# Optimization experiments

Measured on AMD Instinct MI355X. Metric: run time of the kernel, lower is better.

Reference implementation:

```python
import jax, jax.numpy as jnp
import numpy as np

B, T, DIM, H = 2, 2048, 1024, 16
DH = DIM // H  # head dim = 64, rope half = 32


def _apply_rope(q, k):
    # q,k: [b,h,t,d]
    b, h, t, d = q.shape
    half = d // 2
    idx = jnp.arange(half, dtype=jnp.float32)
    pos = jnp.arange(t, dtype=jnp.float32)[:, None]
    inv = 10000.0 ** (-2.0 * idx / (2.0 * half))
    ang = pos * inv  # [t, half]
    cos = jnp.cos(ang).astype(q.dtype)[None, None]  # [1,1,t,half]
    sin = jnp.sin(ang).astype(q.dtype)[None, None]

    def rot(x):
        a = x[..., :half]
        b2 = x[..., half:2 * half]
        return jnp.concatenate([a * cos - b2 * sin, a * sin + b2 * cos], axis=-1)

    return rot(q), rot(k)


def setup_inputs() -> dict:
    key = jax.random.key(0)
    k0, k1, k2 = jax.random.split(key, 3)
    x = jax.random.normal(k0, (B, T, DIM), dtype=jnp.float32)
    mask = jnp.tril(jnp.ones((T, T), dtype=jnp.int32))[None, None]  # causal [1,1,T,T]
    scale = DIM ** -0.5
    W_qkv = jax.random.normal(k1, (DIM, 3 * DIM), dtype=jnp.float32) * scale
    b_qkv = jnp.zeros((3 * DIM,), dtype=jnp.float32)
    W_out = jax.random.normal(k2, (DIM, DIM), dtype=jnp.float32) * scale
    b_out = jnp.zeros((DIM,), dtype=jnp.float32)
    return {"x": x, "mask": mask, "W_qkv": W_qkv, "b_qkv": b_qkv,
            "W_out": W_out, "b_out": b_out}


def reference(x, mask, W_qkv, b_qkv, W_out, b_out):
    b, t, c = x.shape
    qkv = x @ W_qkv + b_qkv  # [b,t,3c]
    q, k, v = jnp.split(qkv, 3, axis=-1)
    q = q.reshape(b, t, H, DH).transpose(0, 2, 1, 3)  # [b,h,t,dh]
    k = k.reshape(b, t, H, DH).transpose(0, 2, 1, 3)
    v = v.reshape(b, t, H, DH).transpose(0, 2, 1, 3)
    q, k = _apply_rope(q, k)
    s = jnp.einsum('bhqd,bhkd->bhqk', q, k) * (DH ** -0.5)
    s = jnp.where(mask == 0, -jnp.inf, s)
    p = jax.nn.softmax(s, axis=-1)  # dropout is identity (drop=0.0)
    y = jnp.einsum('bhqk,bhkd->bhqd', p, v)
    y = y.transpose(0, 2, 1, 3).reshape(b, t, c)
    return y @ W_out + b_out
```

## Files before the change

kernel.cpp:

```cpp
#include <hip/hip_runtime.h>
#include <hip/hip_bf16.h>
#include <math.h>

#define BB 2
#define TT 2048
#define DIMM 1024
#define HH 16
#define DHH 64

typedef _Float16 half8_t __attribute__((ext_vector_type(8)));
typedef _Float16 half4_t __attribute__((ext_vector_type(4)));
typedef float floatx4 __attribute__((ext_vector_type(4)));

typedef const unsigned int __attribute__((address_space(1)))* gp_t;
typedef unsigned int __attribute__((address_space(3)))* lp_t;

__device__ __forceinline__ void async16(const void* g, void* l) {
    __builtin_amdgcn_global_load_lds((gp_t)g, (lp_t)l, 16, 0, 0);
}

template <int CTRL>
__device__ __forceinline__ float dppmov(float x) {
    return __builtin_bit_cast(float, __builtin_amdgcn_update_dpp(
        0, __builtin_bit_cast(int, x), CTRL, 0xf, 0xf, false));
}
__device__ __forceinline__ float rowred_sum(float v) {
    v += dppmov<0x128>(v);
    v += dppmov<0x124>(v);
    v += dppmov<0x122>(v);
    v += dppmov<0x121>(v);
    return v;
}

__global__ __launch_bounds__(256) void prep_kernel(
    const float* __restrict__ x, _Float16* __restrict__ xb,
    const float* __restrict__ W_qkv, _Float16* __restrict__ Wqt,
    const float* __restrict__ W_out, _Float16* __restrict__ Wot,
    float2* __restrict__ tab) {
    __shared__ float tile[32][33];
    int bid = blockIdx.x, tid = threadIdx.x;
    if (bid < 4096) {
        int i = (bid * 256 + tid) * 4;
        floatx4 v = *(const floatx4*)(x + i);
        half4_t h;
        h[0] = (_Float16)v[0]; h[1] = (_Float16)v[1];
        h[2] = (_Float16)v[2]; h[3] = (_Float16)v[3];
        *(half4_t*)(xb + i) = h;
    } else if (bid < 8192) {
        const float* W; _Float16* Wt; int K, N, bx, by;
        if (bid < 7168) {
            W = W_qkv; Wt = Wqt; K = 1024; N = 3072;
            int b2 = bid - 4096; bx = b2 % 96; by = b2 / 96;
        } else {
            W = W_out; Wt = Wot; K = 1024; N = 1024;
            int b2 = bid - 7168; bx = b2 & 31; by = b2 >> 5;
        }
        int n0 = bx * 32, k0 = by * 32;
        int tx = tid & 31, ty = tid >> 5;
        for (int i = 0; i < 32; i += 8)
            tile[ty + i][tx] = W[(size_t)(k0 + ty + i) * N + n0 + tx];
        __syncthreads();
        for (int i = 0; i < 32; i += 8)
            Wt[(size_t)(n0 + ty + i) * K + k0 + tx] = (_Float16)tile[tx][ty + i];
    } else {
        int idx = (bid - 8192) * 256 + tid;
        int t = idx >> 5, d = idx & 31;
        float inv = __expf(-(float)d * 0.28782313662425572f);
        float ang = (float)t * inv;
        float s, c;
        __sincosf(ang, &s, &c);
        tab[idx] = make_float2(c, s);
    }
}

template <int BN, int MODE>
__global__ __launch_bounds__(256) void gemm_ld_kernel(
    const _Float16* __restrict__ A, const _Float16* __restrict__ Bt,
    const float* __restrict__ bias, float* __restrict__ C,
    _Float16* __restrict__ Qr, _Float16* __restrict__ Kr, _Float16* __restrict__ Vt,
    const float2* __restrict__ tab,
    int M, int N, int K) {
    constexpr int NB = (BN == 128) ? 4 : 2;
    constexpr int BCH = BN * 32;
    constexpr int BOFF = 3 * 4096;
    __shared__ __align__(16) _Float16 smem[3 * 4096 + 3 * BCH];
    int tid = threadIdx.x;
    int m0 = blockIdx.y * 128, n0 = blockIdx.x * BN;
    int wave = tid >> 6, lane = tid & 63;
    int wm = (wave & 1) * 64;
    int wn = (wave >> 1) * (BN / 2);
    int lm = lane & 15, quad = lane >> 4;

    floatx4 acc[4][NB] = {};

    int arow = tid >> 2, ach = tid & 3;
    int acol = ((ach ^ (arow & 3)) << 3);

    auto stage = [&](int k0, int buf) {
        _Float16* Ab = smem + buf * 4096;
        _Float16* Bb = smem + BOFF + buf * BCH;
        async16(A + (size_t)(m0 + arow) * K + k0 + acol, (char*)Ab + tid * 16);
        async16(A + (size_t)(m0 + 64 + arow) * K + k0 + acol, (char*)Ab + (256 + tid) * 16);
        async16(Bt + (size_t)(n0 + arow) * K + k0 + acol, (char*)Bb + tid * 16);
        if (BN == 128)
            async16(Bt + (size_t)(n0 + 64 + arow) * K + k0 + acol, (char*)Bb + (256 + tid) * 16);
    };

    int nIt = K >> 5;
    stage(0, 0);
    stage(32, 1);
    int fsw = (quad ^ (lm & 3)) << 3;
    for (int it = 0; it < nIt; ++it) {
        int buf = it % 3;
        if (it < nIt - 1) {
            if (BN == 128) asm volatile("s_waitcnt vmcnt(4)" ::: "memory");
            else           asm volatile("s_waitcnt vmcnt(3)" ::: "memory");
        } else {
            asm volatile("s_waitcnt vmcnt(0)" ::: "memory");
        }
        asm volatile("s_barrier" ::: "memory");
        if (it + 2 < nIt) stage((it + 2) << 5, (it + 2) % 3);

        const _Float16* Ab = smem + buf * 4096;
        const _Float16* Bb = smem + BOFF + buf * BCH;
        half8_t af[4], bf[NB];
        for (int mb = 0; mb < 4; mb++)
            af[mb] = *(const half8_t*)&Ab[(wm + mb * 16 + lm) * 32 + fsw];
        for (int nb = 0; nb < NB; nb++)
            bf[nb] = *(const half8_t*)&Bb[(wn + nb * 16 + lm) * 32 + fsw];
        for (int mb = 0; mb < 4; mb++)
            for (int nb = 0; nb < NB; nb++)
                acc[mb][nb] = __builtin_amdgcn_mfma_f32_16x16x32_f16(af[mb], bf[nb], acc[mb][nb], 0, 0, 0);
    }

    if (MODE == 0) {
        for (int mb = 0; mb < 4; mb++) {
            int row = m0 + wm + mb * 16 + quad * 4;
            for (int nb = 0; nb < NB; nb++) {
                int col = n0 + wn + nb * 16 + lm;
                float bv = bias[col];
                for (int r = 0; r < 4; r++)
                    C[(size_t)(row + r) * N + col] = acc[mb][nb][r] + bv;
            }
        }
    } else {
        __syncthreads();
        _Float16* scratch = smem + wave * 4096;
        int col0 = n0 + wn;
        int sect = col0 >> 10;
        int h = (col0 & 1023) >> 6;
        int b = (m0 + wm) >> 11;
        int tbase = (m0 + wm) & 2047;
        if (sect < 2) {
            _Float16* dst = (sect == 0) ? Qr : Kr;
            float fscale = (sect == 0) ? 0.18033688011112042f : 1.0f;
            for (int nb = 0; nb < 2; nb++) {
                int d = nb * 16 + lm;
                float bva = bias[col0 + d];
                float bvb = bias[col0 + d + 32];
                int d2 = d + 32;
                for (int mb = 0; mb < 4; mb++) {
                    for (int r = 0; r < 4; r++) {
                        int tl = mb * 16 + quad * 4 + r;
                        float2 cs = tab[(tbase + tl) * 32 + d];
                        float va = acc[mb][nb][r] + bva;
                        float vb = acc[mb][nb + 2][r] + bvb;
                        int sw = tl & 7;
                        scratch[tl * 64 + (((d >> 3) ^ sw) << 3) + (d & 7)] =
                            (_Float16)((va * cs.x - vb * cs.y) * fscale);
                        scratch[tl * 64 + (((d2 >> 3) ^ sw) << 3) + (d2 & 7)] =
                            (_Float16)((va * cs.y + vb * cs.x) * fscale);
                    }
                }
            }
            asm volatile("s_waitcnt lgkmcnt(0)" ::: "memory");
            size_t ob = (size_t)(b * HH + h) * TT + tbase;
            for (int j = 0; j < 8; j++) {
                int row = j * 8 + (lane >> 3);
                int c = lane & 7;
                half8_t v = *(const half8_t*)&scratch[row * 64 + ((c ^ (row & 7)) << 3)];
                *(half8_t*)&dst[(ob + row) * 64 + c * 8] = v;
            }
        } else {
            for (int nb = 0; nb < 4; nb++) {
                int d = nb * 16 + lm;
                float bv = bias[col0 + d];
                int sw = d & 7;
                for (int mb = 0; mb < 4; mb++) {
                    int t0 = mb * 16 + quad * 4;
                    half4_t pv;
                    for (int r = 0; r < 4; r++) pv[r] = (_Float16)(acc[mb][nb][r] + bv);
                    *(half4_t*)&scratch[d * 64 + (((t0 >> 3) ^ sw) << 3) + (t0 & 7)] = pv;
                }
            }
            asm volatile("s_waitcnt lgkmcnt(0)" ::: "memory");
            size_t vb0 = (size_t)(b * HH + h) * 64;
            for (int j = 0; j < 8; j++) {
                int drow = j * 8 + (lane >> 3);
                int c = lane & 7;
                half8_t v = *(const half8_t*)&scratch[drow * 64 + ((c ^ (drow & 7)) << 3)];
                *(half8_t*)&Vt[(vb0 + drow) * TT + tbase + c * 8] = v;
            }
        }
    }
}

__global__ __launch_bounds__(512, 2) void qkv_gemm256(
    const _Float16* __restrict__ A, const _Float16* __restrict__ Bt,
    const float* __restrict__ bias,
    _Float16* __restrict__ Qr, _Float16* __restrict__ Kr, _Float16* __restrict__ Vt,
    const float2* __restrict__ tab) {
    constexpr int K = 1024;
    __shared__ __align__(16) _Float16 smem[65536];
    int tid = threadIdx.x;
    int m0 = blockIdx.y * 256, n0 = blockIdx.x * 256;
    int wave = tid >> 6, lane = tid & 63;
    int wm = (wave & 1) * 128;
    int wn = (wave >> 1) * 64;
    int lm = lane & 15, quad = lane >> 4;

    int srow = tid >> 3;
    int sch = (tid & 7) ^ (srow & 7);
    const _Float16* aSrc = A + (size_t)(m0 + srow) * K + sch * 8;
    const _Float16* bSrc = Bt + (size_t)(n0 + srow) * K + sch * 8;

    auto stageA = [&](int kt, int buf) {
        const _Float16* s = aSrc + kt * 64;
        char* d = (char*)smem + buf * 32768 + tid * 16;
#pragma unroll
        for (int i = 0; i < 4; i++)
            async16(s + (size_t)i * 64 * K, d + i * 8192);
    };
    auto stageB = [&](int kt, int buf) {
        const _Float16* s = bSrc + kt * 64;
        char* d = (char*)smem + 65536 + buf * 32768 + tid * 16;
#pragma unroll
        for (int i = 0; i < 4; i++)
            async16(s + (size_t)i * 64 * K, d + i * 8192);
    };

    int ch0 = (quad ^ (lm & 7)) << 3;
    int ch1 = ((4 + quad) ^ (lm & 7)) << 3;

    floatx4 acc[8][4] = {};
    half8_t af[4][2], bf[4][2];

    stageA(0, 0);
    stageB(0, 0);
    asm volatile("s_waitcnt vmcnt(0)" ::: "memory");
    __builtin_amdgcn_s_barrier();

#pragma unroll 2
    for (int kt = 0; kt < 16; ++kt) {
        int c = kt & 1, nbuf = c ^ 1;
        const _Float16* Ap = smem + c * 16384 + (wm + lm) * 64;
        const _Float16* Bp = smem + 32768 + c * 16384 + (wn + lm) * 64;

#pragma unroll
        for (int mf = 0; mf < 4; mf++) {
            af[mf][0] = *(const half8_t*)(Ap + mf * 1024 + ch0);
            af[mf][1] = *(const half8_t*)(Ap + mf * 1024 + ch1);
        }
#pragma unroll
        for (int nf = 0; nf < 2; nf++) {
            bf[nf][0] = *(const half8_t*)(Bp + nf * 1024 + ch0);
            bf[nf][1] = *(const half8_t*)(Bp + nf * 1024 + ch1);
        }
        if (kt < 15) stageA(kt + 1, nbuf);
        __builtin_amdgcn_s_barrier();
        __builtin_amdgcn_s_setprio(1);
#pragma unroll
        for (int mf = 0; mf < 4; mf++)
#pragma unroll
            for (int nf = 0; nf < 2; nf++) {
                acc[mf][nf] = __builtin_amdgcn_mfma_f32_16x16x32_f16(af[mf][0], bf[nf][0], acc[mf][nf], 0, 0, 0);
                acc[mf][nf] = __builtin_amdgcn_mfma_f32_16x16x32_f16(af[mf][1], bf[nf][1], acc[mf][nf], 0, 0, 0);
            }
        __builtin_amdgcn_s_setprio(0);
        __builtin_amdgcn_s_barrier();

#pragma unroll
        for (int nf = 2; nf < 4; nf++) {
            bf[nf][0] = *(const half8_t*)(Bp + nf * 1024 + ch0);
            bf[nf][1] = *(const half8_t*)(Bp + nf * 1024 + ch1);
        }
        if (kt < 15) stageB(kt + 1, nbuf);
        __builtin_amdgcn_s_barrier();
        __builtin_amdgcn_s_setprio(1);
#pragma unroll
        for (int mf = 0; mf < 4; mf++)
#pragma unroll
            for (int nf = 2; nf < 4; nf++) {
                acc[mf][nf] = __builtin_amdgcn_mfma_f32_16x16x32_f16(af[mf][0], bf[nf][0], acc[mf][nf], 0, 0, 0);
                acc[mf][nf] = __builtin_amdgcn_mfma_f32_16x16x32_f16(af[mf][1], bf[nf][1], acc[mf][nf], 0, 0, 0);
            }
        __builtin_amdgcn_s_setprio(0);
        __builtin_amdgcn_s_barrier();

#pragma unroll
        for (int mf = 0; mf < 4; mf++) {
            af[mf][0] = *(const half8_t*)(Ap + (4 + mf) * 1024 + ch0);
            af[mf][1] = *(const half8_t*)(Ap + (4 + mf) * 1024 + ch1);
        }
        __builtin_amdgcn_s_barrier();
        __builtin_amdgcn_s_setprio(1);
#pragma unroll
        for (int mf = 0; mf < 4; mf++)
#pragma unroll
            for (int nf = 2; nf < 4; nf++) {
                acc[4 + mf][nf] = __builtin_amdgcn_mfma_f32_16x16x32_f16(af[mf][0], bf[nf][0], acc[4 + mf][nf], 0, 0, 0);
                acc[4 + mf][nf] = __builtin_amdgcn_mfma_f32_16x16x32_f16(af[mf][1], bf[nf][1], acc[4 + mf][nf], 0, 0, 0);
            }
        __builtin_amdgcn_s_setprio(0);
        __builtin_amdgcn_s_barrier();

        __builtin_amdgcn_s_setprio(1);
#pragma unroll
        for (int mf = 0; mf < 4; mf++)
#pragma unroll
            for (int nf = 0; nf < 2; nf++) {
                acc[4 + mf][nf] = __builtin_amdgcn_mfma_f32_16x16x32_f16(af[mf][0], bf[nf][0], acc[4 + mf][nf], 0, 0, 0);
                acc[4 + mf][nf] = __builtin_amdgcn_mfma_f32_16x16x32_f16(af[mf][1], bf[nf][1], acc[4 + mf][nf], 0, 0, 0);
            }
        __builtin_amdgcn_s_setprio(0);
        asm volatile("s_waitcnt vmcnt(0)" ::: "memory");
        __builtin_amdgcn_s_barrier();
    }

    __syncthreads();
    _Float16* scratch = smem + wave * 8192;
    int col0 = n0 + wn;
    int sect = col0 >> 10;
    int h = (col0 & 1023) >> 6;
    int b = (m0 + wm) >> 11;
    int tbase = (m0 + wm) & 2047;
    if (sect < 2) {
        _Float16* dst = (sect == 0) ? Qr : Kr;
        float fscale = (sect == 0) ? 0.18033688011112042f : 1.0f;
#pragma unroll
        for (int nb = 0; nb < 2; nb++) {
            int d = nb * 16 + lm;
            float bva = bias[col0 + d];
            float bvb = bias[col0 + d + 32];
            int d2 = d + 32;
#pragma unroll
            for (int mf = 0; mf < 8; mf++) {
#pragma unroll
                for (int r = 0; r < 4; r++) {
                    int tl = mf * 16 + quad * 4 + r;
                    float2 cs = tab[(tbase + tl) * 32 + d];
                    float va = acc[mf][nb][r] + bva;
                    float vb = acc[mf][nb + 2][r] + bvb;
                    int sw = tl & 7;
                    scratch[tl * 64 + (((d >> 3) ^ sw) << 3) + (d & 7)] =
                        (_Float16)((va * cs.x - vb * cs.y) * fscale);
                    scratch[tl * 64 + (((d2 >> 3) ^ sw) << 3) + (d2 & 7)] =
                        (_Float16)((va * cs.y + vb * cs.x) * fscale);
                }
            }
        }
        asm volatile("s_waitcnt lgkmcnt(0)" ::: "memory");
        size_t ob = (size_t)(b * HH + h) * TT + tbase;
        for (int j = 0; j < 16; j++) {
            int row = j * 8 + (lane >> 3);
            int c2 = lane & 7;
            half8_t v = *(const half8_t*)&scratch[row * 64 + ((c2 ^ (row & 7)) << 3)];
            *(half8_t*)&dst[(ob + row) * 64 + c2 * 8] = v;
        }
    } else {
#pragma unroll
        for (int nf = 0; nf < 4; nf++) {
            int d = nf * 16 + lm;
            float bv = bias[col0 + d];
            int sw = d & 7;
#pragma unroll
            for (int mf = 0; mf < 8; mf++) {
                int t0 = mf * 16 + quad * 4;
                int tc = t0 >> 3;
                half4_t pv;
#pragma unroll
                for (int r = 0; r < 4; r++) pv[r] = (_Float16)(acc[mf][nf][r] + bv);
                *(half4_t*)&scratch[d * 128 + (((tc & 8) | ((tc & 7) ^ sw)) << 3) + (t0 & 7)] = pv;
            }
        }
        asm volatile("s_waitcnt lgkmcnt(0)" ::: "memory");
        size_t vb0 = (size_t)(b * HH + h) * 64;
        for (int j = 0; j < 16; j++) {
            int drow = j * 4 + (lane >> 4);
            int c2 = lane & 15;
            int ptc = (c2 & 8) | ((c2 & 7) ^ (drow & 7));
            half8_t v = *(const half8_t*)&scratch[drow * 128 + (ptc << 3)];
            *(half8_t*)&Vt[(vb0 + drow) * TT + tbase + c2 * 8] = v;
        }
    }
}

__device__ const unsigned char kBlkMap[24] = {
    30, 28, 26, 24, 22, 20, 18, 16, 14, 31,
    12, 29, 10, 27, 8, 25, 6, 23, 4, 21, 2, 19, 0, 17};

__global__ __launch_bounds__(256, 3) void flash_attn(
    const _Float16* __restrict__ Qr, const _Float16* __restrict__ Kr,
    const _Float16* __restrict__ Vt,
    _Float16* __restrict__ Po, float* __restrict__ Pls, _Float16* __restrict__ Yb) {
    int bh = blockIdx.y;
    int code = kBlkMap[blockIdx.x];
    int iq = code >> 1, ic = code & 1;
    int kstart = ic * 16;
    int kend = min(kstart + 16, 2 * iq + 2);
    bool full = (ic == 0) && (kend == 2 * iq + 2);

    int tid = threadIdx.x, wave = tid >> 6, lane = tid & 63;
    int lm = lane & 15, quad = lane >> 4;
    int q0w = iq * 128 + wave * 32;

    __shared__ __align__(16) _Float16 Ks[2][64 * 64];
    __shared__ __align__(16) _Float16 Vs[2][64 * 64];
    __shared__ __align__(16) _Float16 Pbuf[4][32 * 64];
    _Float16* plds = Pbuf[wave];

    const _Float16* Qbase = Qr + ((size_t)bh * TT + q0w) * 64;
    half8_t aq[2][2];
    for (int mb = 0; mb < 2; mb++) {
        aq[mb][0] = *(const half8_t*)(Qbase + (size_t)(mb * 16 + lm) * 64 + quad * 8);
        aq[mb][1] = *(const half8_t*)(Qbase + (size_t)(mb * 16 + lm) * 64 + 32 + quad * 8);
    }

    const _Float16* Kb = Kr + (size_t)bh * TT * 64;
    const _Float16* Vb = Vt + (size_t)bh * 64 * TT;

    floatx4 o[2][4] = {};
    float lsum[2][4] = {};

    auto stage = [&](int kt, int buf) {
        int k0 = kt * 64;
        for (int i = 0; i < 2; i++) {
            int sl = i * 256 + tid;
            int row = sl >> 3;
            int c = (sl & 7) ^ (row & 7);
            async16(Kb + (size_t)(k0 + row) * 64 + c * 8, (char*)&Ks[buf][0] + sl * 16);
            async16(Vb + (size_t)row * TT + k0 + c * 8, (char*)&Vs[buf][0] + sl * 16);
        }
    };

    stage(kstart, 0);

    for (int kt = kstart; kt < kend; ++kt) {
        int buf = (kt - kstart) & 1;
        __syncthreads();
        if (kt + 1 < kend) stage(kt + 1, buf ^ 1);
        int k0 = kt * 64;
        if (k0 > q0w + 31) continue;

        floatx4 s4[2][4] = {};
        for (int nb = 0; nb < 4; nb++) {
            int row = nb * 16 + lm, sw = row & 7;
            half8_t kb0 = *(const half8_t*)&Ks[buf][row * 64 + ((quad ^ sw) << 3)];
            half8_t kb1 = *(const half8_t*)&Ks[buf][row * 64 + (((4 + quad) ^ sw) << 3)];
            for (int mb = 0; mb < 2; mb++) {
                s4[mb][nb] = __builtin_amdgcn_mfma_f32_16x16x32_f16(aq[mb][0], kb0, s4[mb][nb], 0, 0, 0);
                s4[mb][nb] = __builtin_amdgcn_mfma_f32_16x16x32_f16(aq[mb][1], kb1, s4[mb][nb], 0, 0, 0);
            }
        }

        if (k0 + 63 > q0w) {
            for (int mb = 0; mb < 2; mb++)
                for (int nb = 0; nb < 4; nb++) {
                    int col = k0 + nb * 16 + lm;
                    int rowq = q0w + mb * 16 + quad * 4;
                    for (int r = 0; r < 4; r++)
                        if (col > rowq + r) s4[mb][nb][r] = -1e30f;
                }
        }

        for (int mb = 0; mb < 2; mb++)
            for (int nb = 0; nb < 4; nb++) {
                int cbase = nb * 2 + (lm >> 3);
                for (int r = 0; r < 4; r++) {
                    float p = __builtin_amdgcn_exp2f(s4[mb][nb][r]);
                    lsum[mb][r] += p;
                    int prow = mb * 16 + quad * 4 + r;
                    plds[prow * 64 + ((cbase ^ (prow & 7)) << 3) + (lm & 7)] = (_Float16)p;
                }
            }
        asm volatile("s_waitcnt lgkmcnt(0)" ::: "memory");
        int psw = lm & 7;
        half8_t pa[2][2];
        for (int mp = 0; mp < 2; mp++) {
            pa[mp][0] = *(const half8_t*)&plds[(mp * 16 + lm) * 64 + ((quad ^ psw) << 3)];
            pa[mp][1] = *(const half8_t*)&plds[(mp * 16 + lm) * 64 + (((4 + quad) ^ psw) << 3)];
        }
        asm volatile("" ::: "memory");

        for (int db = 0; db < 4; db++) {
            int row = db * 16 + lm, sw = row & 7;
            half8_t vb0 = *(const half8_t*)&Vs[buf][row * 64 + ((quad ^ sw) << 3)];
            half8_t vb1 = *(const half8_t*)&Vs[buf][row * 64 + (((4 + quad) ^ sw) << 3)];
            for (int mb = 0; mb < 2; mb++) {
                o[mb][db] = __builtin_amdgcn_mfma_f32_16x16x32_f16(pa[mb][0], vb0, o[mb][db], 0, 0, 0);
                o[mb][db] = __builtin_amdgcn_mfma_f32_16x16x32_f16(pa[mb][1], vb1, o[mb][db], 0, 0, 0);
            }
        }
    }

    float lred[2][4];
    for (int mb = 0; mb < 2; mb++)
        for (int r = 0; r < 4; r++)
            lred[mb][r] = rowred_sum(lsum[mb][r]);

    for (int mb = 0; mb < 2; mb++)
        for (int db = 0; db < 4; db++) {
            int cbase = db * 2 + (lm >> 3);
            for (int r = 0; r < 4; r++) {
                int prow = mb * 16 + quad * 4 + r;
                float v = o[mb][db][r];
                if (full) v /= lred[mb][r];
                plds[prow * 64 + ((cbase ^ (prow & 7)) << 3) + (lm & 7)] = (_Float16)v;
            }
        }
    asm volatile("s_waitcnt lgkmcnt(0)" ::: "memory");
    int b = bh >> 4, h = bh & 15;
    size_t pbase = ((size_t)(bh * 16 + iq) * 2 + ic) * 8192;
    for (int j = 0; j < 4; j++) {
        int row = j * 8 + (lane >> 3);
        int c = lane & 7;
        half8_t v = *(const half8_t*)&plds[row * 64 + ((c ^ (row & 7)) << 3)];
        if (full) {
            size_t yb = ((size_t)(b * TT) + iq * 128 + wave * 32 + row) * DIMM + h * 64 + c * 8;
            *(half8_t*)&Yb[yb] = v;
        } else {
            *(half8_t*)&Po[pbase + (wave * 32 + row) * 64 + c * 8] = v;
        }
    }
    if (!full && lm == 0) {
        size_t lb = ((size_t)(bh * 16 + iq) * 2 + ic) * 128;
        for (int mb = 0; mb < 2; mb++)
            for (int r = 0; r < 4; r++)
                Pls[lb + wave * 32 + mb * 16 + quad * 4 + r] = lred[mb][r];
    }
}

__global__ __launch_bounds__(256) void attn_combine(
    const _Float16* __restrict__ Po, const float* __restrict__ Pls,
    _Float16* __restrict__ Yb) {
    int iq = blockIdx.x + 8, bh = blockIdx.y;
    int b = bh >> 4, h = bh & 15;
    int tid = threadIdx.x;
    int row = tid >> 1, cg = (tid & 1) * 32;

    size_t base = ((size_t)(bh * 16 + iq) * 2) * 8192 + row * 64 + cg;
    size_t lb = ((size_t)(bh * 16 + iq) * 2) * 128 + row;
    float l = Pls[lb] + Pls[lb + 128];
    float inv = 1.0f / l;
    const half8_t* p0 = (const half8_t*)&Po[base];
    const half8_t* p1 = (const half8_t*)&Po[base + 8192];
    size_t yb = ((size_t)(b * TT) + iq * 128 + row) * DIMM + h * 64 + cg;
    for (int j = 0; j < 4; j++) {
        half8_t a = p0[j], c = p1[j], v;
        for (int i = 0; i < 8; i++)
            v[i] = (_Float16)(((float)a[i] + (float)c[i]) * inv);
        *(half8_t*)&Yb[yb + j * 8] = v;
    }
}

extern "C" void kernel_launch(void* const* d_in, const int* in_sizes, int n_in,
                              void* d_out, int out_size, void* d_ws, size_t ws_size,
                              hipStream_t stream) {
    const float* x = (const float*)d_in[0];
    const float* W_qkv = (const float*)d_in[2];
    const float* b_qkv = (const float*)d_in[3];
    const float* W_out = (const float*)d_in[4];
    const float* b_out = (const float*)d_in[5];
    float* out = (float*)d_out;

    char* ws = (char*)d_ws;
    _Float16* xb = (_Float16*)ws;   ws += (size_t)4096 * 1024 * 2;
    _Float16* Wqt = (_Float16*)ws;  ws += (size_t)3072 * 1024 * 2;
    _Float16* Wot = (_Float16*)ws;  ws += (size_t)1024 * 1024 * 2;
    _Float16* Qr = (_Float16*)ws;   ws += (size_t)32 * 2048 * 64 * 2;
    _Float16* Kr = (_Float16*)ws;   ws += (size_t)32 * 2048 * 64 * 2;
    _Float16* Vt = (_Float16*)ws;   ws += (size_t)32 * 2048 * 64 * 2;
    _Float16* Yb = (_Float16*)ws;   ws += (size_t)4096 * 1024 * 2;
    float2* tab = (float2*)ws;      ws += (size_t)2048 * 32 * 8;
    _Float16* Po = (_Float16*)ws;   ws += (size_t)32 * 16 * 2 * 8192 * 2;
    float* Pls = (float*)ws;        ws += (size_t)32 * 16 * 2 * 128 * 4;

    prep_kernel<<<8448, 256, 0, stream>>>(x, xb, W_qkv, Wqt, W_out, Wot, tab);

    qkv_gemm256<<<dim3(12, 16), 512, 0, stream>>>(
        xb, Wqt, b_qkv, Qr, Kr, Vt, tab);

    flash_attn<<<dim3(24, 32), 256, 0, stream>>>(Qr, Kr, Vt, Po, Pls, Yb);
    attn_combine<<<dim3(8, 32), 256, 0, stream>>>(Po, Pls, Yb);

    gemm_ld_kernel<64, 0><<<dim3(16, 32), 256, 0, stream>>>(
        Yb, Wot, b_out, out, nullptr, nullptr, nullptr, nullptr, 4096, 1024, 1024);
}
```

Baseline: 189.3 us.

## Split QKV GEMM tile staging into halves with partial vmcnt waits

Restructures the QKV GEMM main loop so the async global-to-LDS loads for the next k-tile are issued in four smaller pieces (two A halves, two B halves). Each piece is gated by a partial s_waitcnt vmcnt instead of a full drain at the end of every iteration, and several barriers are removed. B rows are remapped so each wave loads the rows needed for the next phase first. The aim is more overlap between global loads and MFMA work with fewer stalls, at the cost of fragile vmcnt accounting, where a wrong count could cause a data race.

Result: no change. 187.1 us (-1.1%).

```diff
diff --git a/kernel.cpp b/kernel.cpp
--- a/kernel.cpp
+++ b/kernel.cpp
@@ -1,6 +1,7 @@
 #include <hip/hip_runtime.h>
 #include <hip/hip_bf16.h>
 #include <math.h>
+#include <type_traits>
 
 #define BB 2
 #define TT 2048
@@ -17,6 +18,11 @@
 
 __device__ __forceinline__ void async16(const void* g, void* l) {
     __builtin_amdgcn_global_load_lds((gp_t)g, (lp_t)l, 16, 0, 0);
+}
+
+template <int N>
+__device__ __forceinline__ void vwait() {
+    asm volatile("s_waitcnt vmcnt(%0)" :: "n"(N) : "memory");
 }
 
 template <int CTRL>
@@ -220,23 +226,24 @@
     int lm = lane & 15, quad = lane >> 4;
 
     int srow = tid >> 3;
-    int sch = (tid & 7) ^ (srow & 7);
-    const _Float16* aSrc = A + (size_t)(m0 + srow) * K + sch * 8;
-    const _Float16* bSrc = Bt + (size_t)(n0 + srow) * K + sch * 8;
-
-    auto stageA = [&](int kt, int buf) {
-        const _Float16* s = aSrc + kt * 64;
-        char* d = (char*)smem + buf * 32768 + tid * 16;
-#pragma unroll
-        for (int i = 0; i < 4; i++)
-            async16(s + (size_t)i * 64 * K, d + i * 8192);
+    int sch8 = ((tid & 7) ^ (srow & 7)) << 3;
+
+    auto stageA = [&](int kt, int buf, int half) {
+        const _Float16* s = A + (size_t)(m0 + srow + half * 64) * K + kt * 64 + sch8;
+        char* d = (char*)smem + buf * 32768 + half * 8192 + tid * 16;
+        async16(s, d);
+        async16(s + (size_t)128 * K, d + 16384);
     };
-    auto stageB = [&](int kt, int buf) {
-        const _Float16* s = bSrc + kt * 64;
-        char* d = (char*)smem + 65536 + buf * 32768 + tid * 16;
-#pragma unroll
-        for (int i = 0; i < 4; i++)
-            async16(s + (size_t)i * 64 * K, d + i * 8192);
+    auto stageB = [&](int kt, int buf, int half) {
+#pragma unroll
+        for (int i = 0; i < 2; i++) {
+            int rowbase = (i * 2 + (wave >> 2)) * 64 + half * 32 + (wave & 3) * 8;
+            int row = rowbase + (lane >> 3);
+            const _Float16* s = Bt + (size_t)(n0 + row) * K + kt * 64 +
+                                (((lane & 7) ^ (row & 7)) << 3);
+            char* d = (char*)smem + 65536 + buf * 32768 + rowbase * 128 + lane * 16;
+            async16(s, d);
+        }
     };
 
     int ch0 = (quad ^ (lm & 7)) << 3;
@@ -245,17 +252,19 @@
     floatx4 acc[8][4] = {};
     half8_t af[4][2], bf[4][2];
 
-    stageA(0, 0);
-    stageB(0, 0);
-    asm volatile("s_waitcnt vmcnt(0)" ::: "memory");
-    __builtin_amdgcn_s_barrier();
-
-#pragma unroll 2
-    for (int kt = 0; kt < 16; ++kt) {
-        int c = kt & 1, nbuf = c ^ 1;
-        const _Float16* Ap = smem + c * 16384 + (wm + lm) * 64;
-        const _Float16* Bp = smem + 32768 + c * 16384 + (wn + lm) * 64;
-
+    stageA(0, 0, 0);
+    stageB(0, 0, 0);
+    stageB(0, 0, 1);
+    stageA(0, 0, 1);
+
+    auto tileStep = [&](auto lastc, int kt) {
+        constexpr bool LAST = decltype(lastc)::value;
+        int cb = kt & 1, nb = cb ^ 1;
+        const _Float16* Ap = smem + cb * 16384 + (wm + lm) * 64;
+        const _Float16* Bp = smem + 32768 + cb * 16384 + (wn + lm) * 64;
+
+        vwait<4>();
+        __builtin_amdgcn_s_barrier();
 #pragma unroll
         for (int mf = 0; mf < 4; mf++) {
             af[mf][0] = *(const half8_t*)(Ap + mf * 1024 + ch0);
@@ -266,8 +275,7 @@
             bf[nf][0] = *(const half8_t*)(Bp + nf * 1024 + ch0);
             bf[nf][1] = *(const half8_t*)(Bp + nf * 1024 + ch1);
         }
-        if (kt < 15) stageA(kt + 1, nbuf);
-        __builtin_amdgcn_s_barrier();
+        if constexpr (!LAST) stageA(kt + 1, nb, 0);
         __builtin_amdgcn_s_setprio(1);
 #pragma unroll
         for (int mf = 0; mf < 4; mf++)
@@ -277,15 +285,15 @@
                 acc[mf][nf] = __builtin_amdgcn_mfma_f32_16x16x32_f16(af[mf][1], bf[nf][1], acc[mf][nf], 0, 0, 0);
             }
         __builtin_amdgcn_s_setprio(0);
+
+        vwait<LAST ? 2 : 4>();
         __builtin_amdgcn_s_barrier();
-
 #pragma unroll
         for (int nf = 2; nf < 4; nf++) {
             bf[nf][0] = *(const half8_t*)(Bp + nf * 1024 + ch0);
             bf[nf][1] = *(const half8_t*)(Bp + nf * 1024 + ch1);
         }
-        if (kt < 15) stageB(kt + 1, nbuf);
-        __builtin_amdgcn_s_barrier();
+        if constexpr (!LAST) stageB(kt + 1, nb, 0);
         __builtin_amdgcn_s_setprio(1);
 #pragma unroll
         for (int mf = 0; mf < 4; mf++)
@@ -295,14 +303,15 @@
                 acc[mf][nf] = __builtin_amdgcn_mfma_f32_16x16x32_f16(af[mf][1], bf[nf][1], acc[mf][nf], 0, 0, 0);
             }
         __builtin_amdgcn_s_setprio(0);
+
+        vwait<LAST ? 0 : 4>();
         __builtin_amdgcn_s_barrier();
-
 #pragma unroll
         for (int mf = 0; mf < 4; mf++) {
             af[mf][0] = *(const half8_t*)(Ap + (4 + mf) * 1024 + ch0);
             af[mf][1] = *(const half8_t*)(Ap + (4 + mf) * 1024 + ch1);
         }
-        __builtin_amdgcn_s_barrier();
+        if constexpr (!LAST) stageB(kt + 1, nb, 1);
         __builtin_amdgcn_s_setprio(1);
 #pragma unroll
         for (int mf = 0; mf < 4; mf++)
@@ -312,8 +321,9 @@
                 acc[4 + mf][nf] = __builtin_amdgcn_mfma_f32_16x16x32_f16(af[mf][1], bf[nf][1], acc[4 + mf][nf], 0, 0, 0);
             }
         __builtin_amdgcn_s_setprio(0);
+
         __builtin_amdgcn_s_barrier();
-
+        if constexpr (!LAST) stageA(kt + 1, nb, 1);
         __builtin_amdgcn_s_setprio(1);
 #pragma unroll
         for (int mf = 0; mf < 4; mf++)
@@ -323,9 +333,11 @@
                 acc[4 + mf][nf] = __builtin_amdgcn_mfma_f32_16x16x32_f16(af[mf][1], bf[nf][1], acc[4 + mf][nf], 0, 0, 0);
             }
         __builtin_amdgcn_s_setprio(0);
-        asm volatile("s_waitcnt vmcnt(0)" ::: "memory");
-        __builtin_amdgcn_s_barrier();
-    }
+    };
+
+    for (int kt = 0; kt < 15; ++kt)
+        tileStep(std::integral_constant<bool, false>{}, kt);
+    tileStep(std::integral_constant<bool, true>{}, 15);
 
     __syncthreads();
     _Float16* scratch = smem + wave * 8192;
```
